# Optimization experiments

Hardware: AMD Instinct MI355X
Metric: run time of the kernel (lower is better)

Reference implementation:

```python
import jax, jax.numpy as jnp
import numpy as np

BS, L, D = 32, 512, 512
N_CHARS = 32
DICT = 97

def setup_inputs() -> dict:
    key = jax.random.key(0)
    ks = jax.random.split(key, 10)
    s = 1.0 / np.sqrt(D)
    return {
        "inp": jax.random.normal(ks[0], (BS, L, D), jnp.float32),
        "emb": jax.random.normal(ks[1], (N_CHARS, D), jnp.float32) * 0.02,  # embedding table; char_orders == arange
        "Wo_w": jax.random.normal(ks[2], (D, D), jnp.float32) * s,
        "Wo_b": jnp.zeros((D,), jnp.float32),
        "Wv_w": jax.random.normal(ks[3], (D, D), jnp.float32) * s,
        "Wv_b": jnp.zeros((D,), jnp.float32),
        "We_w": jax.random.normal(ks[4], (D, 1), jnp.float32) * s,
        "We_b": jnp.zeros((1,), jnp.float32),
        "Wc_w": jax.random.normal(ks[5], (D, DICT), jnp.float32) * s,
        "Wc_b": jnp.zeros((DICT,), jnp.float32),
    }

def reference(inp, emb, Wo_w, Wo_b, Wv_w, Wv_b, We_w, We_b, Wc_w, Wc_b):
    # O = embedding(arange(max_n_chars)) is just the full embedding table: (n, d)
    w_o = emb @ Wo_w + Wo_b                      # (n, d)
    w_v = inp @ Wv_w + Wv_b                      # (b, L, d)
    # broadcast add -> tanh -> score projection: (b, n, L, d) -> (b, n, L)
    h = jnp.tanh(w_o[None, :, None, :] + w_v[:, None, :, :])
    e = jnp.einsum('bnld,d->bnl', h, We_w[:, 0]) + We_b[0]
    alpha = jax.nn.softmax(e, axis=2)            # softmax over L (axis=2)
    visual_features = jnp.einsum('bnl,bld->bnd', alpha, inp)  # (b, n, d)
    logits = visual_features @ Wc_w + Wc_b       # (b, n, dict)
    return (visual_features, logits)
```

## Files before the change

kernel.cpp:

```cpp
#include <hip/hip_runtime.h>
#include <hip/hip_bf16.h>

#define BS    32
#define LSEQ  512
#define DIM   512
#define NCH   32
#define NDICT 97
#define CHB   16

#define TANH_SCALE 2.8853900817779268f

typedef __attribute__((ext_vector_type(8))) short bf16x8;
typedef __attribute__((ext_vector_type(4))) float f32x4;

#define GLDS16(gsrc, ldst) \
  __builtin_amdgcn_global_load_lds((const __attribute__((address_space(1))) void*)(gsrc), \
                                   (__attribute__((address_space(3))) void*)(ldst), 16, 0, 0)

__device__ __forceinline__ float sig_from_scaled(float xs) {
    float e2 = __builtin_amdgcn_exp2f(xs);
    return __builtin_amdgcn_rcpf(1.0f + e2);
}

__device__ __forceinline__ void split2u(float x0, float x1, unsigned& hp, unsigned& lp) {
    unsigned r0 = __float_as_uint(x0) + 0x8000u;
    unsigned r1 = __float_as_uint(x1) + 0x8000u;
    float f0 = __uint_as_float(r0 & 0xFFFF0000u);
    float f1 = __uint_as_float(r1 & 0xFFFF0000u);
    hp = (r0 >> 16) | (r1 & 0xFFFF0000u);
    unsigned s0 = __float_as_uint(x0 - f0);
    unsigned s1 = __float_as_uint(x1 - f1);
    lp = (s0 >> 16) | (s1 & 0xFFFF0000u);
}

__global__ __launch_bounds__(256) void k_prep(
    const float* __restrict__ in, ushort* __restrict__ Ahi, ushort* __restrict__ Alo,
    const float* __restrict__ Wv, ushort* __restrict__ BhiT, ushort* __restrict__ BloT,
    const float* __restrict__ Wo, ushort* __restrict__ WohiT, ushort* __restrict__ WoloT,
    const float* __restrict__ emb, ushort* __restrict__ embH, ushort* __restrict__ embL)
{
    __shared__ float tile[64][65];
    const int bid = blockIdx.x;
    const int t = threadIdx.x;
    if (bid < 2048) {
        const int i0 = bid * 1024 + t;
        #pragma unroll
        for (int rep = 0; rep < 4; ++rep) {
            const int i = i0 + rep * 256;
            float4 v = ((const float4*)in)[i];
            unsigned h01, l01, h23, l23;
            split2u(v.x, v.y, h01, l01);
            split2u(v.z, v.w, h23, l23);
            ((uint2*)Ahi)[i] = make_uint2(h01, h23);
            ((uint2*)Alo)[i] = make_uint2(l01, l23);
        }
    } else if (bid < 2176) {
        const bool isWv = bid < 2112;
        const float* src = isWv ? Wv : Wo;
        ushort* dH = isWv ? BhiT : WohiT;
        ushort* dL = isWv ? BloT : WoloT;
        const int bb = (bid - 2048) & 63;
        const int k0 = (bb >> 3) * 64, n0 = (bb & 7) * 64;
        const int tr = t >> 4, tc = (t & 15) * 4;
        #pragma unroll
        for (int rr = 0; rr < 64; rr += 16) {
            float4 v = *(const float4*)&src[(size_t)(k0 + rr + tr) * DIM + n0 + tc];
            tile[rr + tr][tc + 0] = v.x; tile[rr + tr][tc + 1] = v.y;
            tile[rr + tr][tc + 2] = v.z; tile[rr + tr][tc + 3] = v.w;
        }
        __syncthreads();
        #pragma unroll
        for (int rr = 0; rr < 64; rr += 16) {
            const int n = rr + tr;
            unsigned h01, l01, h23, l23;
            split2u(tile[tc + 0][n] * TANH_SCALE, tile[tc + 1][n] * TANH_SCALE, h01, l01);
            split2u(tile[tc + 2][n] * TANH_SCALE, tile[tc + 3][n] * TANH_SCALE, h23, l23);
            *(uint2*)&dH[(size_t)(n0 + n) * DIM + k0 + tc] = make_uint2(h01, h23);
            *(uint2*)&dL[(size_t)(n0 + n) * DIM + k0 + tc] = make_uint2(l01, l23);
        }
    } else {
        for (int i = t; i < 4096; i += 256) {
            float4 v = ((const float4*)emb)[i];
            unsigned h01, l01, h23, l23;
            split2u(v.x, v.y, h01, l01);
            split2u(v.z, v.w, h23, l23);
            ((uint2*)embH)[i] = make_uint2(h01, h23);
            ((uint2*)embL)[i] = make_uint2(l01, l23);
        }
    }
}

__global__ __launch_bounds__(256) void k_gemm(
    const ushort* __restrict__ Ahi, const ushort* __restrict__ Alo,
    const ushort* __restrict__ Bhi, const ushort* __restrict__ Blo,
    const float* __restrict__ bias, float* __restrict__ C,
    const ushort* __restrict__ WohiT, const ushort* __restrict__ WoloT,
    const ushort* __restrict__ embH, const ushort* __restrict__ embL,
    const float* __restrict__ Wo_b, float* __restrict__ w_o)
{
    __shared__ ushort AhS[8192], AlS[8192], BhS[8192], BlS[8192];

    const int bid = blockIdx.x;
    const int t = threadIdx.x;
    const int wave = t >> 6, lane = t & 63;

    const int srow = lane >> 2;
    const int sg   = (lane & 3) ^ ((lane >> 3) & 3);
    const int fr   = lane & 15;
    const int fswz = ((lane >> 4) ^ ((fr >> 1) & 3)) * 8;

    if (bid < 512) {
        const int mb = (bid & 7) * 16 + (bid >> 5);
        const int nb = (bid >> 3) & 3;
        const int bm = mb * 128, bn = nb * 128;
        const int wm = wave >> 1, wn = wave & 1;
        const int arow0 = (wm * 64 + fr) * 32;
        const int brow0 = (wn * 64 + fr) * 32;

        f32x4 acc[4][4] = {};

        auto stage = [&](int p, int k0) {
            #pragma unroll
            for (int c2 = 0; c2 < 2; ++c2) {
                const int c = wave * 2 + c2;
                const size_t ga = (size_t)(bm + c * 16 + srow) * DIM + k0 + sg * 8;
                const size_t gb = (size_t)(bn + c * 16 + srow) * DIM + k0 + sg * 8;
                GLDS16(Ahi + ga, &AhS[p * 4096 + c * 512]);
                GLDS16(Alo + ga, &AlS[p * 4096 + c * 512]);
                GLDS16(Bhi + gb, &BhS[p * 4096 + c * 512]);
                GLDS16(Blo + gb, &BlS[p * 4096 + c * 512]);
            }
        };

        stage(0, 0);
        __syncthreads();
        int cur = 0;
        for (int ks = 0; ks < 16; ++ks) {
            if (ks < 15) stage(cur ^ 1, (ks + 1) * 32);
            const int co = cur * 4096;
            bf16x8 ah[4], al[4], bh[4], bl[4];
            #pragma unroll
            for (int i = 0; i < 4; ++i) {
                ah[i] = *(const bf16x8*)&AhS[co + arow0 + i * 512 + fswz];
                al[i] = *(const bf16x8*)&AlS[co + arow0 + i * 512 + fswz];
                bh[i] = *(const bf16x8*)&BhS[co + brow0 + i * 512 + fswz];
                bl[i] = *(const bf16x8*)&BlS[co + brow0 + i * 512 + fswz];
            }
            #pragma unroll
            for (int i = 0; i < 4; ++i)
                #pragma unroll
                for (int j = 0; j < 4; ++j) {
                    acc[i][j] = __builtin_amdgcn_mfma_f32_16x16x32_bf16(ah[i], bh[j], acc[i][j], 0, 0, 0);
                    acc[i][j] = __builtin_amdgcn_mfma_f32_16x16x32_bf16(ah[i], bl[j], acc[i][j], 0, 0, 0);
                    acc[i][j] = __builtin_amdgcn_mfma_f32_16x16x32_bf16(al[i], bh[j], acc[i][j], 0, 0, 0);
                }
            __syncthreads();
            cur ^= 1;
        }

        #pragma unroll
        for (int i = 0; i < 4; ++i) {
            const int m = bm + wm * 64 + i * 16 + (lane >> 4) * 4;
            #pragma unroll
            for (int j = 0; j < 4; ++j) {
                const int n = bn + wn * 64 + j * 16 + fr;
                const float bb = TANH_SCALE * bias[n];
                #pragma unroll
                for (int r = 0; r < 4; ++r)
                    C[(size_t)(m + r) * DIM + n] = acc[i][j][r] + bb;
            }
        }
    } else {
        const int nb0 = (bid - 512) * 128;
        const int crow0 = (wave * 32 + fr) * 32;
        f32x4 acc[2][2] = {};

        for (int k0 = 0; k0 < DIM; k0 += 32) {
            #pragma unroll
            for (int c4 = 0; c4 < 4; ++c4) {
                const int idx = wave * 4 + c4;
                const int pl = idx & 1, c = idx >> 1;
                const size_t gb = (size_t)(nb0 + c * 16 + srow) * DIM + k0 + sg * 8;
                if (pl) { GLDS16(WoloT + gb, &BlS[c * 512]); }
                else    { GLDS16(WohiT + gb, &BhS[c * 512]); }
            }
            bf16x8 eh[2], el[2];
            #pragma unroll
            for (int m = 0; m < 2; ++m) {
                const size_t ra = (size_t)(m * 16 + fr) * DIM + k0 + (lane >> 4) * 8;
                eh[m] = *(const bf16x8*)&embH[ra];
                el[m] = *(const bf16x8*)&embL[ra];
            }
            __syncthreads();

            bf16x8 bh[2], bl[2];
            #pragma unroll
            for (int j = 0; j < 2; ++j) {
                bh[j] = *(const bf16x8*)&BhS[crow0 + j * 512 + fswz];
                bl[j] = *(const bf16x8*)&BlS[crow0 + j * 512 + fswz];
            }
            #pragma unroll
            for (int m = 0; m < 2; ++m)
                #pragma unroll
                for (int j = 0; j < 2; ++j) {
                    acc[m][j] = __builtin_amdgcn_mfma_f32_16x16x32_bf16(eh[m], bh[j], acc[m][j], 0, 0, 0);
                    acc[m][j] = __builtin_amdgcn_mfma_f32_16x16x32_bf16(eh[m], bl[j], acc[m][j], 0, 0, 0);
                    acc[m][j] = __builtin_amdgcn_mfma_f32_16x16x32_bf16(el[m], bh[j], acc[m][j], 0, 0, 0);
                }
            __syncthreads();
        }

        #pragma unroll
        for (int m = 0; m < 2; ++m) {
            const int row = m * 16 + (lane >> 4) * 4;
            #pragma unroll
            for (int j = 0; j < 2; ++j) {
                const int col = nb0 + wave * 32 + j * 16 + fr;
                const float bb = TANH_SCALE * Wo_b[col];
                #pragma unroll
                for (int r = 0; r < 4; ++r)
                    w_o[(size_t)(row + r) * DIM + col] = acc[m][j][r] + bb;
            }
        }
    }
}

__global__ __launch_bounds__(256, 4) void k_e(
    const float* __restrict__ w_v, const float* __restrict__ w_o,
    const float* __restrict__ We_w, float* __restrict__ e)
{
    __shared__ float4 woS[CHB * 128];
    const int lblk = blockIdx.x;
    const int b    = blockIdx.y;
    const int ch0  = blockIdx.z * CHB;
    const int t    = threadIdx.x;

    const float4* wog = ((const float4*)w_o) + ch0 * (DIM / 4);
    #pragma unroll
    for (int i = 0; i < CHB * 128 / 256; ++i)
        woS[t + 256 * i] = wog[t + 256 * i];

    const int wave = t >> 6, lane = t & 63;
    const int g = lane >> 4, j = lane & 15;
    const int l = lblk * 16 + wave * 4 + g;

    const float4* wvp = (const float4*)(w_v + (size_t)(b * LSEQ + l) * DIM);
    const float4* wep = (const float4*)We_w;
    float4 wv[8], we[8];
    #pragma unroll
    for (int k = 0; k < 8; ++k) {
        wv[k] = wvp[16 * k + j];
        we[k] = wep[16 * k + j];
    }
    float wsum = 0.0f;
    #pragma unroll
    for (int k = 0; k < 8; ++k)
        wsum += (we[k].x + we[k].y) + (we[k].z + we[k].w);
    #pragma unroll
    for (int off = 1; off < 16; off <<= 1) wsum += __shfl_xor(wsum, off, 64);

    __syncthreads();

    float sv[CHB];
    #pragma unroll 4
    for (int i = 0; i < CHB; ++i) {
        const float4* wrow = &woS[i * 128];
        float s0 = 0.f, s1 = 0.f, s2 = 0.f, s3 = 0.f;
        #pragma unroll
        for (int k = 0; k < 8; ++k) {
            float4 wo4 = wrow[16 * k + j];
            s0 = fmaf(we[k].x, sig_from_scaled(wo4.x + wv[k].x), s0);
            s1 = fmaf(we[k].y, sig_from_scaled(wo4.y + wv[k].y), s1);
            s2 = fmaf(we[k].z, sig_from_scaled(wo4.z + wv[k].z), s2);
            s3 = fmaf(we[k].w, sig_from_scaled(wo4.w + wv[k].w), s3);
        }
        sv[i] = (s0 + s1) + (s2 + s3);
    }

    float t2[8];
    #pragma unroll
    for (int i = 0; i < 8; ++i) {
        float a = sv[2 * i]     + __shfl_xor(sv[2 * i],     1, 64);
        float c = sv[2 * i + 1] + __shfl_xor(sv[2 * i + 1], 1, 64);
        t2[i] = (j & 1) ? c : a;
    }
    float t4[4];
    #pragma unroll
    for (int i = 0; i < 4; ++i) {
        float a = t2[2 * i]     + __shfl_xor(t2[2 * i],     2, 64);
        float c = t2[2 * i + 1] + __shfl_xor(t2[2 * i + 1], 2, 64);
        t4[i] = (j & 2) ? c : a;
    }
    float t8[2];
    #pragma unroll
    for (int i = 0; i < 2; ++i) {
        float a = t4[2 * i]     + __shfl_xor(t4[2 * i],     4, 64);
        float c = t4[2 * i + 1] + __shfl_xor(t4[2 * i + 1], 4, 64);
        t8[i] = (j & 4) ? c : a;
    }
    float a = t8[0] + __shfl_xor(t8[0], 8, 64);
    float c = t8[1] + __shfl_xor(t8[1], 8, 64);
    float res = (j & 8) ? c : a;

    e[(size_t)(b * NCH + ch0 + j) * LSEQ + l] = fmaf(-2.0f, res, wsum);
}

__global__ __launch_bounds__(256) void k_soft(
    const float* __restrict__ e, ushort* __restrict__ aH, ushort* __restrict__ aL)
{
    const int row = blockIdx.x * 4 + (threadIdx.x >> 6);
    const int lane = threadIdx.x & 63;
    const float4* erow = (const float4*)(e + (size_t)row * LSEQ);
    float4 v0 = erow[2 * lane], v1 = erow[2 * lane + 1];
    float m = fmaxf(fmaxf(fmaxf(v0.x, v0.y), fmaxf(v0.z, v0.w)),
                    fmaxf(fmaxf(v1.x, v1.y), fmaxf(v1.z, v1.w)));
    #pragma unroll
    for (int off = 32; off > 0; off >>= 1) m = fmaxf(m, __shfl_xor(m, off, 64));
    float p[8];
    p[0] = __expf(v0.x - m); p[1] = __expf(v0.y - m);
    p[2] = __expf(v0.z - m); p[3] = __expf(v0.w - m);
    p[4] = __expf(v1.x - m); p[5] = __expf(v1.y - m);
    p[6] = __expf(v1.z - m); p[7] = __expf(v1.w - m);
    float s = ((p[0] + p[1]) + (p[2] + p[3])) + ((p[4] + p[5]) + (p[6] + p[7]));
    #pragma unroll
    for (int off = 32; off > 0; off >>= 1) s += __shfl_xor(s, off, 64);
    const float inv = 1.0f / s;
    unsigned h01, l01, h23, l23, h45, l45, h67, l67;
    split2u(p[0] * inv, p[1] * inv, h01, l01);
    split2u(p[2] * inv, p[3] * inv, h23, l23);
    split2u(p[4] * inv, p[5] * inv, h45, l45);
    split2u(p[6] * inv, p[7] * inv, h67, l67);
    uint2* oh = (uint2*)(aH + (size_t)row * LSEQ);
    uint2* ol = (uint2*)(aL + (size_t)row * LSEQ);
    oh[2 * lane]     = make_uint2(h01, h23);
    oh[2 * lane + 1] = make_uint2(h45, h67);
    ol[2 * lane]     = make_uint2(l01, l23);
    ol[2 * lane + 1] = make_uint2(l45, l67);
}

__global__ __launch_bounds__(256) void k_vf(
    const float* __restrict__ inp,
    const ushort* __restrict__ aH, const ushort* __restrict__ aL,
    float* __restrict__ part)
{
    __shared__ unsigned T[4][16 * 68];
    const int dgrp = blockIdx.x >> 1, ls = blockIdx.x & 1;
    const int b = blockIdx.y;
    const int t = threadIdx.x, wave = t >> 6, lane = t & 63;
    const int d0 = (dgrp * 4 + wave) * 16;
    const int lbase = ls * 256;
    const int c = lane & 15, g = lane >> 4;

    unsigned* Tw = T[wave];
    const ushort* aHb = aH + (size_t)b * NCH * LSEQ;
    const ushort* aLb = aL + (size_t)b * NCH * LSEQ;

    f32x4 acc0 = {}, acc1 = {};

    for (int l0 = 0; l0 < 256; l0 += 64) {
        const float4* src = (const float4*)(inp + ((size_t)(b * LSEQ) + lbase + l0 + lane) * DIM + d0);
        float4 v0 = src[0], v1 = src[1], v2 = src[2], v3 = src[3];
        unsigned ev[16];
        {
            unsigned hp, lp;
            split2u(v0.x, v0.y, hp, lp); ev[0] = (lp << 16) | (hp & 0xFFFFu); ev[1] = (lp & 0xFFFF0000u) | (hp >> 16);
            split2u(v0.z, v0.w, hp, lp); ev[2] = (lp << 16) | (hp & 0xFFFFu); ev[3] = (lp & 0xFFFF0000u) | (hp >> 16);
            split2u(v1.x, v1.y, hp, lp); ev[4] = (lp << 16) | (hp & 0xFFFFu); ev[5] = (lp & 0xFFFF0000u) | (hp >> 16);
            split2u(v1.z, v1.w, hp, lp); ev[6] = (lp << 16) | (hp & 0xFFFFu); ev[7] = (lp & 0xFFFF0000u) | (hp >> 16);
            split2u(v2.x, v2.y, hp, lp); ev[8] = (lp << 16) | (hp & 0xFFFFu); ev[9] = (lp & 0xFFFF0000u) | (hp >> 16);
            split2u(v2.z, v2.w, hp, lp); ev[10] = (lp << 16) | (hp & 0xFFFFu); ev[11] = (lp & 0xFFFF0000u) | (hp >> 16);
            split2u(v3.x, v3.y, hp, lp); ev[12] = (lp << 16) | (hp & 0xFFFFu); ev[13] = (lp & 0xFFFF0000u) | (hp >> 16);
            split2u(v3.z, v3.w, hp, lp); ev[14] = (lp << 16) | (hp & 0xFFFFu); ev[15] = (lp & 0xFFFF0000u) | (hp >> 16);
        }
        #pragma unroll
        for (int i = 0; i < 16; ++i)
            Tw[i * 68 + lane] = ev[i];
        #pragma unroll
        for (int ks = 0; ks < 2; ++ks) {
            const unsigned* bp = &Tw[c * 68 + ks * 32 + g * 8];
            uint4 w0 = *(const uint4*)bp;
            uint4 w1 = *(const uint4*)(bp + 4);
            union { unsigned u[4]; bf16x8 v; } H, L;
            H.u[0] = (w0.x & 0xFFFFu) | (w0.y << 16);
            H.u[1] = (w0.z & 0xFFFFu) | (w0.w << 16);
            H.u[2] = (w1.x & 0xFFFFu) | (w1.y << 16);
            H.u[3] = (w1.z & 0xFFFFu) | (w1.w << 16);
            L.u[0] = (w0.x >> 16) | (w0.y & 0xFFFF0000u);
            L.u[1] = (w0.z >> 16) | (w0.w & 0xFFFF0000u);
            L.u[2] = (w1.x >> 16) | (w1.y & 0xFFFF0000u);
            L.u[3] = (w1.z >> 16) | (w1.w & 0xFFFF0000u);

            const int lfrag = lbase + l0 + ks * 32 + g * 8;
            bf16x8 a0h = *(const bf16x8*)&aHb[(size_t)c * LSEQ + lfrag];
            bf16x8 a0l = *(const bf16x8*)&aLb[(size_t)c * LSEQ + lfrag];
            bf16x8 a1h = *(const bf16x8*)&aHb[(size_t)(16 + c) * LSEQ + lfrag];
            bf16x8 a1l = *(const bf16x8*)&aLb[(size_t)(16 + c) * LSEQ + lfrag];

            acc0 = __builtin_amdgcn_mfma_f32_16x16x32_bf16(a0h, H.v, acc0, 0, 0, 0);
            acc0 = __builtin_amdgcn_mfma_f32_16x16x32_bf16(a0h, L.v, acc0, 0, 0, 0);
            acc0 = __builtin_amdgcn_mfma_f32_16x16x32_bf16(a0l, H.v, acc0, 0, 0, 0);
            acc1 = __builtin_amdgcn_mfma_f32_16x16x32_bf16(a1h, H.v, acc1, 0, 0, 0);
            acc1 = __builtin_amdgcn_mfma_f32_16x16x32_bf16(a1h, L.v, acc1, 0, 0, 0);
            acc1 = __builtin_amdgcn_mfma_f32_16x16x32_bf16(a1l, H.v, acc1, 0, 0, 0);
        }
    }

    const size_t base = (size_t)(ls * BS * NCH + b * NCH) * DIM + d0 + c;
    #pragma unroll
    for (int r = 0; r < 4; ++r) {
        part[base + (size_t)(g * 4 + r) * DIM]        = acc0[r];
        part[base + (size_t)(16 + g * 4 + r) * DIM]   = acc1[r];
    }
}

__global__ __launch_bounds__(256) void k_lg(
    const float* __restrict__ part, const float* __restrict__ Wc_w,
    const float* __restrict__ Wc_b, float* __restrict__ out_vf,
    float* __restrict__ out_logits)
{
    __shared__ float vfS[4][DIM];
    __shared__ float lgS[2][4][NDICT];
    const int r0 = blockIdx.x * 4;
    const int t = threadIdx.x;
    const int wave = t >> 6, lane = t & 63;

    const float2* p0 = (const float2*)(part + (size_t)(r0 + wave) * DIM);
    const float2* p1 = (const float2*)(part + (size_t)(BS * NCH + r0 + wave) * DIM);
    float2* vout = (float2*)(out_vf + (size_t)(r0 + wave) * DIM);
    #pragma unroll
    for (int q = 0; q < 4; ++q) {
        float2 x = p0[lane + 64 * q], y = p1[lane + 64 * q];
        float2 z; z.x = x.x + y.x; z.y = x.y + y.y;
        ((float2*)&vfS[wave][0])[lane + 64 * q] = z;
        vout[lane + 64 * q] = z;
    }
    __syncthreads();

    const int j = t & 127, half = t >> 7;
    if (j < NDICT) {
        const float* wc = Wc_w + (size_t)half * 256 * NDICT + j;
        const float* v0 = &vfS[0][half * 256];
        const float* v1 = &vfS[1][half * 256];
        const float* v2 = &vfS[2][half * 256];
        const float* v3 = &vfS[3][half * 256];
        float a0 = 0.f, a1 = 0.f, a2 = 0.f, a3 = 0.f;
        #pragma unroll 4
        for (int d = 0; d < 256; ++d) {
            float w = wc[(size_t)d * NDICT];
            a0 = fmaf(v0[d], w, a0); a1 = fmaf(v1[d], w, a1);
            a2 = fmaf(v2[d], w, a2); a3 = fmaf(v3[d], w, a3);
        }
        lgS[half][0][j] = a0; lgS[half][1][j] = a1;
        lgS[half][2][j] = a2; lgS[half][3][j] = a3;
    }
    __syncthreads();
    for (int idx = t; idx < 4 * NDICT; idx += 256) {
        const int r = idx / NDICT, jj = idx - r * NDICT;
        out_logits[(size_t)(r0 + r) * NDICT + jj] = Wc_b[jj] + lgS[0][r][jj] + lgS[1][r][jj];
    }
}

extern "C" void kernel_launch(void* const* d_in, const int* in_sizes, int n_in,
                              void* d_out, int out_size, void* d_ws, size_t ws_size,
                              hipStream_t stream)
{
    const float* inp  = (const float*)d_in[0];
    const float* emb  = (const float*)d_in[1];
    const float* Wo_w = (const float*)d_in[2];
    const float* Wo_b = (const float*)d_in[3];
    const float* Wv_w = (const float*)d_in[4];
    const float* Wv_b = (const float*)d_in[5];
    const float* We_w = (const float*)d_in[6];
    const float* Wc_w = (const float*)d_in[8];
    const float* Wc_b = (const float*)d_in[9];

    char* p = (char*)d_ws;
    float*  w_o   = (float*)p;  p += (64 << 10);
    float*  ev    = (float*)p;  p += (size_t)BS * NCH * LSEQ * 4;
    ushort* BhiT  = (ushort*)p; p += (size_t)DIM * DIM * 2;
    ushort* BloT  = (ushort*)p; p += (size_t)DIM * DIM * 2;
    ushort* WohiT = (ushort*)p; p += (size_t)DIM * DIM * 2;
    ushort* WoloT = (ushort*)p; p += (size_t)DIM * DIM * 2;
    ushort* embH  = (ushort*)p; p += (size_t)NCH * DIM * 2;
    ushort* embL  = (ushort*)p; p += (size_t)NCH * DIM * 2;
    ushort* aH    = (ushort*)p; p += (size_t)BS * NCH * LSEQ * 2;
    ushort* aL    = (ushort*)p; p += (size_t)BS * NCH * LSEQ * 2;
    float*  partV = (float*)p;  p += (size_t)2 * BS * NCH * DIM * 4;
    ushort* Ahi   = (ushort*)p; p += (size_t)BS * LSEQ * DIM * 2;
    ushort* Alo   = (ushort*)p; p += (size_t)BS * LSEQ * DIM * 2;
    float*  w_v   = (float*)p;

    float* out_vf = (float*)d_out;
    float* out_lg = out_vf + BS * NCH * DIM;

    k_prep<<<dim3(2177), dim3(256), 0, stream>>>(inp, Ahi, Alo, Wv_w, BhiT, BloT,
                                                 Wo_w, WohiT, WoloT, emb, embH, embL);
    k_gemm<<<dim3(516), dim3(256), 0, stream>>>(Ahi, Alo, BhiT, BloT, Wv_b, w_v,
                                                WohiT, WoloT, embH, embL, Wo_b, w_o);
    k_e<<<dim3(LSEQ / 16, BS, NCH / CHB), dim3(256), 0, stream>>>(w_v, w_o, We_w, ev);
    k_soft<<<dim3(256), dim3(256), 0, stream>>>(ev, aH, aL);
    k_vf<<<dim3(16, BS), dim3(256), 0, stream>>>(inp, aH, aL, partV);
    k_lg<<<dim3(256), dim3(256), 0, stream>>>(partV, Wc_w, Wc_b, out_vf, out_lg);
}
```

Measured before the change: 152.6 us.

## Fuse fp32-to-bf16 hi/lo split of input into GEMM A-tile loading

The prep kernel no longer converts the large input tensor into separate bf16 hi/lo arrays. Instead, the GEMM stages fp32 A tiles into LDS with a new swizzle and splits them into hi/lo fragments in registers just before the MFMAs. This removes a full write and re-read of the hi/lo copies of the 32MB input. The cost is extra ALU work in the GEMM inner loop and a larger fp32 A tile in LDS. Separately, the logits kernel now handles 8 rows per block instead of 4, halving its grid.

```diff
diff --git a/kernel.cpp b/kernel.cpp
--- a/kernel.cpp
+++ b/kernel.cpp
@@ -34,7 +34,6 @@
 }
 
 __global__ __launch_bounds__(256) void k_prep(
-    const float* __restrict__ in, ushort* __restrict__ Ahi, ushort* __restrict__ Alo,
     const float* __restrict__ Wv, ushort* __restrict__ BhiT, ushort* __restrict__ BloT,
     const float* __restrict__ Wo, ushort* __restrict__ WohiT, ushort* __restrict__ WoloT,
     const float* __restrict__ emb, ushort* __restrict__ embH, ushort* __restrict__ embL)
@@ -42,24 +41,12 @@
     __shared__ float tile[64][65];
     const int bid = blockIdx.x;
     const int t = threadIdx.x;
-    if (bid < 2048) {
-        const int i0 = bid * 1024 + t;
-        #pragma unroll
-        for (int rep = 0; rep < 4; ++rep) {
-            const int i = i0 + rep * 256;
-            float4 v = ((const float4*)in)[i];
-            unsigned h01, l01, h23, l23;
-            split2u(v.x, v.y, h01, l01);
-            split2u(v.z, v.w, h23, l23);
-            ((uint2*)Ahi)[i] = make_uint2(h01, h23);
-            ((uint2*)Alo)[i] = make_uint2(l01, l23);
-        }
-    } else if (bid < 2176) {
-        const bool isWv = bid < 2112;
+    if (bid < 128) {
+        const bool isWv = bid < 64;
         const float* src = isWv ? Wv : Wo;
         ushort* dH = isWv ? BhiT : WohiT;
         ushort* dL = isWv ? BloT : WoloT;
-        const int bb = (bid - 2048) & 63;
+        const int bb = bid & 63;
         const int k0 = (bb >> 3) * 64, n0 = (bb & 7) * 64;
         const int tr = t >> 4, tc = (t & 15) * 4;
         #pragma unroll
@@ -91,44 +78,50 @@
 }
 
 __global__ __launch_bounds__(256) void k_gemm(
-    const ushort* __restrict__ Ahi, const ushort* __restrict__ Alo,
+    const float* __restrict__ A,
     const ushort* __restrict__ Bhi, const ushort* __restrict__ Blo,
     const float* __restrict__ bias, float* __restrict__ C,
     const ushort* __restrict__ WohiT, const ushort* __restrict__ WoloT,
     const ushort* __restrict__ embH, const ushort* __restrict__ embL,
     const float* __restrict__ Wo_b, float* __restrict__ w_o)
 {
-    __shared__ ushort AhS[8192], AlS[8192], BhS[8192], BlS[8192];
+    __shared__ float  AfS[2 * 128 * 32];
+    __shared__ ushort BhS[2 * 128 * 32];
+    __shared__ ushort BlS[2 * 128 * 32];
 
     const int bid = blockIdx.x;
     const int t = threadIdx.x;
     const int wave = t >> 6, lane = t & 63;
 
-    const int srow = lane >> 2;
-    const int sg   = (lane & 3) ^ ((lane >> 3) & 3);
+    const int sgB = (lane & 3) ^ ((lane >> 3) & 3);
+    const int sgA = (lane & 7) ^ ((lane >> 3) & 7);
+
     const int fr   = lane & 15;
-    const int fswz = ((lane >> 4) ^ ((fr >> 1) & 3)) * 8;
+    const int q    = lane >> 4;
+    const int fswzB = (q ^ ((fr >> 1) & 3)) * 8;
 
     if (bid < 512) {
         const int mb = (bid & 7) * 16 + (bid >> 5);
         const int nb = (bid >> 3) & 3;
         const int bm = mb * 128, bn = nb * 128;
         const int wm = wave >> 1, wn = wave & 1;
-        const int arow0 = (wm * 64 + fr) * 32;
         const int brow0 = (wn * 64 + fr) * 32;
+        const int pA0 = (2 * q) ^ (fr & 7);
+        const int pA1 = (2 * q + 1) ^ (fr & 7);
 
         f32x4 acc[4][4] = {};
 
         auto stage = [&](int p, int k0) {
             #pragma unroll
-            for (int c2 = 0; c2 < 2; ++c2) {
-                const int c = wave * 2 + c2;
-                const size_t ga = (size_t)(bm + c * 16 + srow) * DIM + k0 + sg * 8;
-                const size_t gb = (size_t)(bn + c * 16 + srow) * DIM + k0 + sg * 8;
-                GLDS16(Ahi + ga, &AhS[p * 4096 + c * 512]);
-                GLDS16(Alo + ga, &AlS[p * 4096 + c * 512]);
-                GLDS16(Bhi + gb, &BhS[p * 4096 + c * 512]);
-                GLDS16(Blo + gb, &BlS[p * 4096 + c * 512]);
+            for (int c4 = 0; c4 < 4; ++c4) {
+                const int ca = wave * 4 + c4;
+                const size_t ga = (size_t)(bm + ca * 8 + (lane >> 3)) * DIM + k0 + sgA * 4;
+                GLDS16(A + ga, &AfS[p * 4096 + ca * 256]);
+                const int idx = wave * 4 + c4;
+                const int pl = idx & 1, cb = idx >> 1;
+                const size_t gb = (size_t)(bn + cb * 16 + (lane >> 2)) * DIM + k0 + sgB * 8;
+                if (pl) { GLDS16(Blo + gb, &BlS[p * 4096 + cb * 512]); }
+                else    { GLDS16(Bhi + gb, &BhS[p * 4096 + cb * 512]); }
             }
         };
 
@@ -141,10 +134,17 @@
             bf16x8 ah[4], al[4], bh[4], bl[4];
             #pragma unroll
             for (int i = 0; i < 4; ++i) {
-                ah[i] = *(const bf16x8*)&AhS[co + arow0 + i * 512 + fswz];
-                al[i] = *(const bf16x8*)&AlS[co + arow0 + i * 512 + fswz];
-                bh[i] = *(const bf16x8*)&BhS[co + brow0 + i * 512 + fswz];
-                bl[i] = *(const bf16x8*)&BlS[co + brow0 + i * 512 + fswz];
+                const float* arow = &AfS[co + (wm * 64 + i * 16 + fr) * 32];
+                float4 fa = *(const float4*)&arow[pA0 * 4];
+                float4 fb = *(const float4*)&arow[pA1 * 4];
+                union { unsigned u[4]; bf16x8 v; } H, L;
+                split2u(fa.x, fa.y, H.u[0], L.u[0]);
+                split2u(fa.z, fa.w, H.u[1], L.u[1]);
+                split2u(fb.x, fb.y, H.u[2], L.u[2]);
+                split2u(fb.z, fb.w, H.u[3], L.u[3]);
+                ah[i] = H.v; al[i] = L.v;
+                bh[i] = *(const bf16x8*)&BhS[co + brow0 + i * 512 + fswzB];
+                bl[i] = *(const bf16x8*)&BlS[co + brow0 + i * 512 + fswzB];
             }
             #pragma unroll
             for (int i = 0; i < 4; ++i)
@@ -160,7 +160,7 @@
 
         #pragma unroll
         for (int i = 0; i < 4; ++i) {
-            const int m = bm + wm * 64 + i * 16 + (lane >> 4) * 4;
+            const int m = bm + wm * 64 + i * 16 + q * 4;
             #pragma unroll
             for (int j = 0; j < 4; ++j) {
                 const int n = bn + wn * 64 + j * 16 + fr;
@@ -180,14 +180,14 @@
             for (int c4 = 0; c4 < 4; ++c4) {
                 const int idx = wave * 4 + c4;
                 const int pl = idx & 1, c = idx >> 1;
-                const size_t gb = (size_t)(nb0 + c * 16 + srow) * DIM + k0 + sg * 8;
+                const size_t gb = (size_t)(nb0 + c * 16 + (lane >> 2)) * DIM + k0 + sgB * 8;
                 if (pl) { GLDS16(WoloT + gb, &BlS[c * 512]); }
                 else    { GLDS16(WohiT + gb, &BhS[c * 512]); }
             }
             bf16x8 eh[2], el[2];
             #pragma unroll
             for (int m = 0; m < 2; ++m) {
-                const size_t ra = (size_t)(m * 16 + fr) * DIM + k0 + (lane >> 4) * 8;
+                const size_t ra = (size_t)(m * 16 + fr) * DIM + k0 + q * 8;
                 eh[m] = *(const bf16x8*)&embH[ra];
                 el[m] = *(const bf16x8*)&embL[ra];
             }
@@ -196,8 +196,8 @@
             bf16x8 bh[2], bl[2];
             #pragma unroll
             for (int j = 0; j < 2; ++j) {
-                bh[j] = *(const bf16x8*)&BhS[crow0 + j * 512 + fswz];
-                bl[j] = *(const bf16x8*)&BlS[crow0 + j * 512 + fswz];
+                bh[j] = *(const bf16x8*)&BhS[crow0 + j * 512 + fswzB];
+                bl[j] = *(const bf16x8*)&BlS[crow0 + j * 512 + fswzB];
             }
             #pragma unroll
             for (int m = 0; m < 2; ++m)
@@ -212,7 +212,7 @@
 
         #pragma unroll
         for (int m = 0; m < 2; ++m) {
-            const int row = m * 16 + (lane >> 4) * 4;
+            const int row = m * 16 + q * 4;
             #pragma unroll
             for (int j = 0; j < 2; ++j) {
                 const int col = nb0 + wave * 32 + j * 16 + fr;
@@ -418,43 +418,44 @@
     const float* __restrict__ Wc_b, float* __restrict__ out_vf,
     float* __restrict__ out_logits)
 {
-    __shared__ float vfS[4][DIM];
-    __shared__ float lgS[2][4][NDICT];
-    const int r0 = blockIdx.x * 4;
+    __shared__ float vfS[8][DIM];
+    __shared__ float lgS[2][8][NDICT];
+    const int r0 = blockIdx.x * 8;
     const int t = threadIdx.x;
     const int wave = t >> 6, lane = t & 63;
 
-    const float2* p0 = (const float2*)(part + (size_t)(r0 + wave) * DIM);
-    const float2* p1 = (const float2*)(part + (size_t)(BS * NCH + r0 + wave) * DIM);
-    float2* vout = (float2*)(out_vf + (size_t)(r0 + wave) * DIM);
-    #pragma unroll
-    for (int q = 0; q < 4; ++q) {
-        float2 x = p0[lane + 64 * q], y = p1[lane + 64 * q];
-        float2 z; z.x = x.x + y.x; z.y = x.y + y.y;
-        ((float2*)&vfS[wave][0])[lane + 64 * q] = z;
-        vout[lane + 64 * q] = z;
+    #pragma unroll
+    for (int rr = 0; rr < 2; ++rr) {
+        const int row = wave * 2 + rr;
+        const float2* p0 = (const float2*)(part + (size_t)(r0 + row) * DIM);
+        const float2* p1 = (const float2*)(part + (size_t)(BS * NCH + r0 + row) * DIM);
+        float2* vout = (float2*)(out_vf + (size_t)(r0 + row) * DIM);
+        #pragma unroll
+        for (int qq = 0; qq < 4; ++qq) {
+            float2 x = p0[lane + 64 * qq], y = p1[lane + 64 * qq];
+            float2 z; z.x = x.x + y.x; z.y = x.y + y.y;
+            ((float2*)&vfS[row][0])[lane + 64 * qq] = z;
+            vout[lane + 64 * qq] = z;
+        }
     }
     __syncthreads();
 
     const int j = t & 127, half = t >> 7;
     if (j < NDICT) {
         const float* wc = Wc_w + (size_t)half * 256 * NDICT + j;
-        const float* v0 = &vfS[0][half * 256];
-        const float* v1 = &vfS[1][half * 256];
-        const float* v2 = &vfS[2][half * 256];
-        const float* v3 = &vfS[3][half * 256];
-        float a0 = 0.f, a1 = 0.f, a2 = 0.f, a3 = 0.f;
-        #pragma unroll 4
+        float a[8] = {0.f, 0.f, 0.f, 0.f, 0.f, 0.f, 0.f, 0.f};
+        #pragma unroll 2
         for (int d = 0; d < 256; ++d) {
             float w = wc[(size_t)d * NDICT];
-            a0 = fmaf(v0[d], w, a0); a1 = fmaf(v1[d], w, a1);
-            a2 = fmaf(v2[d], w, a2); a3 = fmaf(v3[d], w, a3);
-        }
-        lgS[half][0][j] = a0; lgS[half][1][j] = a1;
-        lgS[half][2][j] = a2; lgS[half][3][j] = a3;
+            #pragma unroll
+            for (int r = 0; r < 8; ++r)
+                a[r] = fmaf(vfS[r][half * 256 + d], w, a[r]);
+        }
+        #pragma unroll
+        for (int r = 0; r < 8; ++r) lgS[half][r][j] = a[r];
     }
     __syncthreads();
-    for (int idx = t; idx < 4 * NDICT; idx += 256) {
+    for (int idx = t; idx < 8 * NDICT; idx += 256) {
         const int r = idx / NDICT, jj = idx - r * NDICT;
         out_logits[(size_t)(r0 + r) * NDICT + jj] = Wc_b[jj] + lgS[0][r][jj] + lgS[1][r][jj];
     }
@@ -486,19 +487,17 @@
     ushort* aH    = (ushort*)p; p += (size_t)BS * NCH * LSEQ * 2;
     ushort* aL    = (ushort*)p; p += (size_t)BS * NCH * LSEQ * 2;
     float*  partV = (float*)p;  p += (size_t)2 * BS * NCH * DIM * 4;
-    ushort* Ahi   = (ushort*)p; p += (size_t)BS * LSEQ * DIM * 2;
-    ushort* Alo   = (ushort*)p; p += (size_t)BS * LSEQ * DIM * 2;
     float*  w_v   = (float*)p;
 
     float* out_vf = (float*)d_out;
     float* out_lg = out_vf + BS * NCH * DIM;
 
-    k_prep<<<dim3(2177), dim3(256), 0, stream>>>(inp, Ahi, Alo, Wv_w, BhiT, BloT,
-                                                 Wo_w, WohiT, WoloT, emb, embH, embL);
-    k_gemm<<<dim3(516), dim3(256), 0, stream>>>(Ahi, Alo, BhiT, BloT, Wv_b, w_v,
+    k_prep<<<dim3(129), dim3(256), 0, stream>>>(Wv_w, BhiT, BloT, Wo_w, WohiT, WoloT,
+                                                emb, embH, embL);
+    k_gemm<<<dim3(516), dim3(256), 0, stream>>>(inp, BhiT, BloT, Wv_b, w_v,
                                                 WohiT, WoloT, embH, embL, Wo_b, w_o);
     k_e<<<dim3(LSEQ / 16, BS, NCH / CHB), dim3(256), 0, stream>>>(w_v, w_o, We_w, ev);
     k_soft<<<dim3(256), dim3(256), 0, stream>>>(ev, aH, aL);
     k_vf<<<dim3(16, BS), dim3(256), 0, stream>>>(inp, aH, aL, partV);
-    k_lg<<<dim3(256), dim3(256), 0, stream>>>(partV, Wc_w, Wc_b, out_vf, out_lg);
-}
+    k_lg<<<dim3(128), dim3(256), 0, stream>>>(partV, Wc_w, Wc_b, out_vf, out_lg);
+}
```

After: 159.3 us. 4.4% more time.
